# Performance work log

Measured on AMD Instinct MI355X. Metric: run time of the kernel, lower is better.

Reference implementation:

```python
import jax, jax.numpy as jnp
import numpy as np

N, C, E, Q, H, NC = 50000, 128, 1600000, 500000, 256, 2
BN_EPS = 1e-5


def gru_step(x, h, wih, whh, bih, bhh):
    # single-step torch.nn.GRU, gate order (r, z, n); x,h: [C, C] rows as batch
    gi = x @ wih.T + bih
    gh = h @ whh.T + bhh
    ir, iz, inn = jnp.split(gi, 3, axis=-1)
    hr, hz, hn = jnp.split(gh, 3, axis=-1)
    r = jax.nn.sigmoid(ir + hr)
    z = jax.nn.sigmoid(iz + hz)
    n = jnp.tanh(inn + r * hn)
    return (1.0 - z) * n + z * h


def gcn_conv(x, w, src, dst, ew):
    # GCNConv with fixed weight w and symmetric gcn_norm incl. self-loops
    xw = x @ w
    deg = jnp.zeros((N,), xw.dtype).at[dst].add(ew) + 1.0  # +1 self-loop
    dinv = jax.lax.rsqrt(deg)
    norm = dinv[src] * ew * dinv[dst]
    out = jnp.zeros_like(xw).at[dst].add(xw[src] * norm[:, None])
    return out + xw * (dinv * dinv)[:, None]  # self-loop contribution


def evolve_gcno(x, src, dst, ew, w_init, wih, whh, bih, bhh):
    w = gru_step(w_init, w_init, wih, whh, bih, bhh)
    return gcn_conv(x, w, src, dst, ew)


def setup_inputs():
    key = jax.random.key(0)
    ks = jax.random.split(key, 40)
    inp = {}
    inp["X"] = jax.random.normal(ks[0], (N, C), jnp.float32)
    inp["edge_index"] = jax.random.randint(ks[1], (2, E), 0, N, jnp.int32)
    inp["edge_weight"] = jax.random.uniform(ks[2], (E,), jnp.float32)
    inp["edge1"] = jax.random.randint(ks[3], (Q,), 0, N, jnp.int32)
    inp["edge2"] = jax.random.randint(ks[4], (Q,), 0, N, jnp.int32)
    s = 1.0 / np.sqrt(C)
    i = 5
    for l in range(2):
        inp[f"w{l}_init"] = jax.random.uniform(ks[i], (C, C), jnp.float32, -s, s); i += 1
        inp[f"w{l}_ih"] = jax.random.uniform(ks[i], (3 * C, C), jnp.float32, -s, s); i += 1
        inp[f"w{l}_hh"] = jax.random.uniform(ks[i], (3 * C, C), jnp.float32, -s, s); i += 1
        inp[f"b{l}_ih"] = jax.random.uniform(ks[i], (3 * C,), jnp.float32, -s, s); i += 1
        inp[f"b{l}_hh"] = jax.random.uniform(ks[i], (3 * C,), jnp.float32, -s, s); i += 1
    dims = [(H, C), (H, H), (NC, H)]
    for l, (o, fi) in enumerate(dims):
        sl = 1.0 / np.sqrt(fi)
        inp[f"lin_w{l}"] = jax.random.uniform(ks[i], (o, fi), jnp.float32, -sl, sl); i += 1
        inp[f"lin_b{l}"] = jax.random.uniform(ks[i], (o,), jnp.float32, -sl, sl); i += 1
    for l in range(2):
        inp[f"bn_g{l}"] = jax.random.uniform(ks[i], (H,), jnp.float32, 0.5, 1.5); i += 1
        inp[f"bn_b{l}"] = 0.1 * jax.random.normal(ks[i], (H,), jnp.float32); i += 1
        inp[f"bn_m{l}"] = 0.1 * jax.random.normal(ks[i], (H,), jnp.float32); i += 1
        inp[f"bn_v{l}"] = jax.random.uniform(ks[i], (H,), jnp.float32, 0.5, 1.5); i += 1
    return inp


def reference(X, edge_index, edge_weight, edge1, edge2,
              w0_init, w0_ih, w0_hh, b0_ih, b0_hh,
              w1_init, w1_ih, w1_hh, b1_ih, b1_hh,
              lin_w0, lin_b0, lin_w1, lin_b1, lin_w2, lin_b2,
              bn_g0, bn_b0, bn_m0, bn_v0, bn_g1, bn_b1, bn_m1, bn_v1):
    src, dst = edge_index[0], edge_index[1]
    # EGCNO: two EvolveGCNO layers + relu (dropout is identity in eval)
    x = jax.nn.relu(evolve_gcno(X, src, dst, edge_weight, w0_init, w0_ih, w0_hh, b0_ih, b0_hh))
    x = jax.nn.relu(evolve_gcno(x, src, dst, edge_weight, w1_init, w1_ih, w1_hh, b1_ih, b1_hh))
    # edge pair gather + hadamard
    h = x[edge1] * x[edge2]  # [Q, C]
    bn = [(bn_g0, bn_b0, bn_m0, bn_v0), (bn_g1, bn_b1, bn_m1, bn_v1)]
    lins = [(lin_w0, lin_b0), (lin_w1, lin_b1)]
    for (w, b), (g, bb, m, v) in zip(lins, bn):
        h = h @ w.T + b
        h = g * (h - m) * jax.lax.rsqrt(v + BN_EPS) + bb  # BatchNorm1d (eval)
        h = jax.nn.relu(h)
    h = h @ lin_w2.T + lin_b2
    return jax.nn.log_softmax(h, axis=-1)
```

## Files before the change

kernel.cpp:

```cpp
#include <hip/hip_runtime.h>
#include <math.h>

#define N_NODES 50000
#define C_DIM   128
#define E_EDGES 1600000
#define Q_PAIRS 500000
#define H_DIM   256
#define N_CLS   2
#define BN_EPS  1e-5f

typedef __attribute__((ext_vector_type(8))) short bf16x8;
typedef __attribute__((ext_vector_type(4))) short s16x4;
typedef __attribute__((ext_vector_type(4))) unsigned short u16x4;
typedef __attribute__((ext_vector_type(4))) float f32x4;

#define VMCNT0 asm volatile("s_waitcnt vmcnt(0)" ::: "memory")
#define VMCNT1 asm volatile("s_waitcnt vmcnt(1)" ::: "memory")
#define VMCNT2 asm volatile("s_waitcnt vmcnt(2)" ::: "memory")
#define SBAR do { __builtin_amdgcn_s_barrier(); \
                  __builtin_amdgcn_sched_barrier(0); } while (0)

#define DEG_SCALE 2097152.0f

__device__ __forceinline__ unsigned short f2bf(float x) {
    unsigned u = __float_as_uint(x);
    u += 0x7fffu + ((u >> 16) & 1u);
    return (unsigned short)(u >> 16);
}
__device__ __forceinline__ float bf2f(unsigned short h) {
    return __uint_as_float(((unsigned)h) << 16);
}
__device__ __forceinline__ unsigned cvtpk(float a, float b) {
    unsigned r;
    asm("v_cvt_pk_bf16_f32 %0, %1, %2" : "=v"(r) : "v"(a), "v"(b));
    return r;
}

__global__ __launch_bounds__(256) void k_hist(const int* __restrict__ dst,
                                              const float* __restrict__ ew,
                                              unsigned long long* dpack) {
    int e = blockIdx.x * 256 + threadIdx.x;
    if (e < E_EDGES) {
        unsigned pv = __float2uint_rn(ew[e] * DEG_SCALE);
        atomicAdd(&dpack[dst[e]], (1ULL << 32) | (unsigned long long)pv);
    }
}

__global__ __launch_bounds__(1024) void k_scan1(const unsigned long long* __restrict__ dpack,
                                                int* __restrict__ pos,
                                                int* __restrict__ bsum) {
    __shared__ int pa[1024], pb[1024];
    int t = threadIdx.x;
    int x = blockIdx.x * 1024 + t;
    int v = (x < N_NODES) ? (int)(dpack[x] >> 32) : 0;
    pa[t] = v;
    __syncthreads();
    int* sp = pa; int* dp = pb;
    for (int o = 1; o < 1024; o <<= 1) {
        int u = sp[t] + ((t >= o) ? sp[t - o] : 0);
        dp[t] = u;
        __syncthreads();
        int* tmp = sp; sp = dp; dp = tmp;
    }
    if (x < N_NODES) pos[x] = sp[t];
    if (t == 1023) bsum[blockIdx.x] = sp[1023];
}
__global__ __launch_bounds__(64) void k_scan2(const int* __restrict__ bsum,
                                              int* __restrict__ boff) {
    int t = threadIdx.x;
    int v = (t < 49) ? bsum[t] : 0;
    int own = v;
    for (int o = 1; o < 64; o <<= 1) {
        int u = __shfl_up(v, o, 64);
        if (t >= o) v += u;
    }
    if (t < 49) boff[t] = v - own;
}
__global__ __launch_bounds__(1024) void k_scan3(const unsigned long long* __restrict__ dpack,
                                                int* __restrict__ pos,
                                                const int* __restrict__ boff,
                                                int* __restrict__ off,
                                                float* __restrict__ dinv) {
    int x = blockIdx.x * 1024 + threadIdx.x;
    if (x >= N_NODES) return;
    int c = (int)(dpack[x] >> 32);
    int incl = pos[x];
    int o = boff[blockIdx.x] + incl - c;
    off[x] = o;
    pos[x] = o;
    if (x == N_NODES - 1) off[N_NODES] = o + c;
    unsigned lo = (unsigned)(dpack[x] & 0xffffffffULL);
    dinv[x] = rsqrtf(1.0f + (float)lo * (1.0f / DEG_SCALE));
}

__global__ __launch_bounds__(256) void k_fill(const int* __restrict__ src,
                                              const int* __restrict__ dst,
                                              const float* __restrict__ ew,
                                              const float* __restrict__ dinv,
                                              int* pos,
                                              int2* __restrict__ csr) {
    int e = blockIdx.x * 256 + threadIdx.x;
    if (e >= E_EDGES) return;
    int s = src[e], d = dst[e];
    int slot = atomicAdd(&pos[d], 1);
    int2 p;
    p.x = s;
    p.y = __float_as_int(dinv[s] * ew[e] * dinv[d]);
    csr[slot] = p;
}

__global__ __launch_bounds__(256) void k_gru_xbf(
    const float* __restrict__ wi0, const float* __restrict__ wih0, const float* __restrict__ whh0,
    const float* __restrict__ bih0, const float* __restrict__ bhh0, float* __restrict__ we0,
    const float* __restrict__ wi1, const float* __restrict__ wih1, const float* __restrict__ whh1,
    const float* __restrict__ bih1, const float* __restrict__ bhh1, float* __restrict__ we1,
    const float* __restrict__ x, unsigned short* __restrict__ xb) {
    if (blockIdx.x < 256) {
        __shared__ float xrow[C_DIM];
        int layer = blockIdx.x >> 7;
        int i = blockIdx.x & 127, j = threadIdx.x;
        const float* w_init = layer ? wi1 : wi0;
        const float* wih = layer ? wih1 : wih0;
        const float* whh = layer ? whh1 : whh0;
        const float* bih = layer ? bih1 : bih0;
        const float* bhh = layer ? bhh1 : bhh0;
        float* w_out = layer ? we1 : we0;
        if (j < C_DIM) xrow[j] = w_init[i * C_DIM + j];
        __syncthreads();
        if (j < C_DIM) {
            float gi[3], gh[3];
#pragma unroll
            for (int g = 0; g < 3; ++g) {
                const float* wi = wih + (size_t)(g * C_DIM + j) * C_DIM;
                const float* wh = whh + (size_t)(g * C_DIM + j) * C_DIM;
                float ai = 0.f, ah = 0.f;
                for (int k = 0; k < C_DIM; ++k) { ai += xrow[k] * wi[k]; ah += xrow[k] * wh[k]; }
                gi[g] = ai + bih[g * C_DIM + j];
                gh[g] = ah + bhh[g * C_DIM + j];
            }
            float r = 1.f / (1.f + expf(-(gi[0] + gh[0])));
            float z = 1.f / (1.f + expf(-(gi[1] + gh[1])));
            float n = tanhf(gi[2] + r * gh[2]);
            w_out[i * C_DIM + j] = (1.f - z) * n + z * xrow[j];
        }
    } else {
        int i = ((blockIdx.x - 256) * 256 + threadIdx.x) * 8;
        f32x4 a = *(const f32x4*)(x + i);
        f32x4 b = *(const f32x4*)(x + i + 4);
        bf16x8 o;
#pragma unroll
        for (int e = 0; e < 4; ++e) { o[e] = (short)f2bf(a[e]); o[e + 4] = (short)f2bf(b[e]); }
        *(bf16x8*)(xb + i) = o;
    }
}

__global__ __launch_bounds__(256) void k_prep_all(
    const float* __restrict__ we0, const float* __restrict__ we1,
    unsigned short* __restrict__ Wc0, unsigned short* __restrict__ Wc1,
    const float* __restrict__ lw0, const float* __restrict__ lw1,
    unsigned short* __restrict__ W0p, unsigned short* __restrict__ W1p,
    const float* __restrict__ lb0, const float* __restrict__ bg0, const float* __restrict__ bb0,
    const float* __restrict__ bm0, const float* __restrict__ bv0,
    const float* __restrict__ lb1, const float* __restrict__ bg1, const float* __restrict__ bb1,
    const float* __restrict__ bm1, const float* __restrict__ bv1,
    float* __restrict__ shift0, float* __restrict__ shift1) {
    int b = blockIdx.x, t = threadIdx.x;
    if (b < 256) {
        int idx = b * 256 + t;
        int e = idx & 7, col = (idx >> 3) & 127, kg = (idx >> 10) & 3;
        int plane = (idx >> 12) & 1, kb = (idx >> 13) & 3, layer = idx >> 15;
        int k = kb * 32 + kg * 8 + e;
        const float* we = layer ? we1 : we0;
        float x = we[(size_t)k * C_DIM + col];
        unsigned short hi = f2bf(x);
        unsigned short o = plane ? f2bf(x - bf2f(hi)) : hi;
        (layer ? Wc1 : Wc0)[idx & 32767] = o;
    } else if (b < 384) {
        int idx = (b - 256) * 256 + t;
        int e = idx & 7, col = (idx >> 3) & 255, kg = (idx >> 11) & 3;
        int kb = idx >> 13;
        int k = kb * 32 + kg * 8 + e;
        float sc = bg0[col] * rsqrtf(bv0[col] + BN_EPS);
        W0p[idx] = f2bf(lw0[(size_t)col * C_DIM + k] * sc);
    } else if (b < 640) {
        int idx = (b - 384) * 256 + t;
        int e = idx & 7, col = (idx >> 3) & 255, kg = (idx >> 11) & 3;
        int kb = idx >> 13;
        int k = kb * 32 + kg * 8 + e;
        float sc = bg1[col] * rsqrtf(bv1[col] + BN_EPS);
        W1p[idx] = f2bf(lw1[(size_t)col * H_DIM + k] * sc);
    } else {
        int j = (b - 640) * 256 + t;
        if (j < 256) {
            float sc = bg0[j] * rsqrtf(bv0[j] + BN_EPS);
            shift0[j] = (lb0[j] - bm0[j]) * sc + bb0[j];
        } else {
            int i = j - 256;
            float sc = bg1[i] * rsqrtf(bv1[i] + BN_EPS);
            shift1[i] = (lb1[i] - bm1[i]) * sc + bb1[i];
        }
    }
}

__global__ __launch_bounds__(256) void k_agg(const unsigned short* __restrict__ xb,
                                             const float* __restrict__ dinv,
                                             const int* __restrict__ off,
                                             const int2* __restrict__ csr,
                                             float* __restrict__ agg) {
    int tid = blockIdx.x * 256 + threadIdx.x;
    int n = tid >> 5;
    int c = (tid & 31) << 2;
    float dv = dinv[n];
    float d2 = dv * dv;
    u16x4 xs = *(const u16x4*)(xb + (size_t)n * C_DIM + c);
    float4 acc;
    acc.x = d2 * bf2f(xs[0]); acc.y = d2 * bf2f(xs[1]);
    acc.z = d2 * bf2f(xs[2]); acc.w = d2 * bf2f(xs[3]);
    int i = off[n], e = off[n + 1];
    for (; i + 8 <= e; i += 8) {
        int2 q0 = csr[i], q1 = csr[i + 1], q2 = csr[i + 2], q3 = csr[i + 3];
        int2 q4 = csr[i + 4], q5 = csr[i + 5], q6 = csr[i + 6], q7 = csr[i + 7];
        u16x4 v0 = *(const u16x4*)(xb + (size_t)q0.x * C_DIM + c);
        u16x4 v1 = *(const u16x4*)(xb + (size_t)q1.x * C_DIM + c);
        u16x4 v2 = *(const u16x4*)(xb + (size_t)q2.x * C_DIM + c);
        u16x4 v3 = *(const u16x4*)(xb + (size_t)q3.x * C_DIM + c);
        u16x4 v4 = *(const u16x4*)(xb + (size_t)q4.x * C_DIM + c);
        u16x4 v5 = *(const u16x4*)(xb + (size_t)q5.x * C_DIM + c);
        u16x4 v6 = *(const u16x4*)(xb + (size_t)q6.x * C_DIM + c);
        u16x4 v7 = *(const u16x4*)(xb + (size_t)q7.x * C_DIM + c);
        float w0 = __int_as_float(q0.y), w1 = __int_as_float(q1.y);
        float w2 = __int_as_float(q2.y), w3 = __int_as_float(q3.y);
        float w4 = __int_as_float(q4.y), w5 = __int_as_float(q5.y);
        float w6 = __int_as_float(q6.y), w7 = __int_as_float(q7.y);
        acc.x += w0 * bf2f(v0[0]) + w1 * bf2f(v1[0]) + w2 * bf2f(v2[0]) + w3 * bf2f(v3[0])
               + w4 * bf2f(v4[0]) + w5 * bf2f(v5[0]) + w6 * bf2f(v6[0]) + w7 * bf2f(v7[0]);
        acc.y += w0 * bf2f(v0[1]) + w1 * bf2f(v1[1]) + w2 * bf2f(v2[1]) + w3 * bf2f(v3[1])
               + w4 * bf2f(v4[1]) + w5 * bf2f(v5[1]) + w6 * bf2f(v6[1]) + w7 * bf2f(v7[1]);
        acc.z += w0 * bf2f(v0[2]) + w1 * bf2f(v1[2]) + w2 * bf2f(v2[2]) + w3 * bf2f(v3[2])
               + w4 * bf2f(v4[2]) + w5 * bf2f(v5[2]) + w6 * bf2f(v6[2]) + w7 * bf2f(v7[2]);
        acc.w += w0 * bf2f(v0[3]) + w1 * bf2f(v1[3]) + w2 * bf2f(v2[3]) + w3 * bf2f(v3[3])
               + w4 * bf2f(v4[3]) + w5 * bf2f(v5[3]) + w6 * bf2f(v6[3]) + w7 * bf2f(v7[3]);
    }
    for (; i < e; ++i) {
        int2 pe = csr[i];
        float w = __int_as_float(pe.y);
        u16x4 v = *(const u16x4*)(xb + (size_t)pe.x * C_DIM + c);
        acc.x += w * bf2f(v[0]); acc.y += w * bf2f(v[1]);
        acc.z += w * bf2f(v[2]); acc.w += w * bf2f(v[3]);
    }
    *(float4*)(agg + (size_t)n * C_DIM + c) = acc;
}

template <int OUT_BF>
__global__ __launch_bounds__(512) void k_gemm(const float* __restrict__ agg,
                                              const unsigned short* __restrict__ Wc,
                                              float* __restrict__ y,
                                              unsigned short* __restrict__ yb) {
    __shared__ __align__(16) char smem[3 * 8192];
    const int t = threadIdx.x, lane = t & 63, wave = t >> 6;
    const int qg = wave >> 1, ch = wave & 1;
    const int l16 = lane & 15, kg = lane >> 4;
    const int qrow = qg * 16 + l16;
    const int node = blockIdx.x * 64 + qrow;
    const int nodec = node < N_NODES ? node : N_NODES - 1;

    auto STG = [&](int sidx, int b) {
        const char* g = (const char*)Wc + sidx * 8192 + wave * 1024 + lane * 16;
        char* d = smem + b * 8192 + wave * 1024;
        __builtin_amdgcn_global_load_lds((const __attribute__((address_space(1))) void*)g,
                                         (__attribute__((address_space(3))) void*)d, 16, 0, 0);
    };
    STG(0, 0); STG(1, 1);

    bf16x8 bh[4], bl[4];
    const float* ar = agg + (size_t)nodec * C_DIM;
#pragma unroll
    for (int kb = 0; kb < 4; ++kb) {
        int k0 = kb * 32 + kg * 8;
        f32x4 a0 = *(const f32x4*)(ar + k0);
        f32x4 a1 = *(const f32x4*)(ar + k0 + 4);
#pragma unroll
        for (int e = 0; e < 4; ++e) {
            unsigned short h0 = f2bf(a0[e]);
            bh[kb][e] = (short)h0; bl[kb][e] = (short)f2bf(a0[e] - bf2f(h0));
            unsigned short h1 = f2bf(a1[e]);
            bh[kb][e + 4] = (short)h1; bl[kb][e + 4] = (short)f2bf(a1[e] - bf2f(h1));
        }
    }
    f32x4 acc[4];
#pragma unroll
    for (int i = 0; i < 4; ++i) acc[i] = 0.f;

#pragma unroll
    for (int s = 0; s < 8; ++s) {
        if (s < 7) { VMCNT1; } else { VMCNT0; }
        SBAR;
        if (s + 2 < 8) STG(s + 2, (s + 2) % 3);
        const unsigned short* strip = (const unsigned short*)(smem + (s % 3) * 8192);
        const int kb = s >> 1;
        __builtin_amdgcn_s_setprio(1);
#pragma unroll
        for (int jc8 = 0; jc8 < 4; ++jc8) {
            int col = (ch * 4 + jc8) * 16 + l16;
            bf16x8 a = *(const bf16x8*)&strip[kg * 1024 + col * 8];
            acc[jc8] = __builtin_amdgcn_mfma_f32_16x16x32_bf16(a, bh[kb], acc[jc8], 0, 0, 0);
            if ((s & 1) == 0)
                acc[jc8] = __builtin_amdgcn_mfma_f32_16x16x32_bf16(a, bl[kb], acc[jc8], 0, 0, 0);
        }
        __builtin_amdgcn_s_setprio(0);
    }

    if (node < N_NODES) {
#pragma unroll
        for (int jc8 = 0; jc8 < 4; ++jc8) {
            int j0 = (ch * 4 + jc8) * 16 + kg * 4;
            if (OUT_BF) {
                u16x4 v;
#pragma unroll
                for (int r = 0; r < 4; ++r) v[r] = f2bf(fmaxf(acc[jc8][r], 0.f));
                *(u16x4*)(yb + (size_t)node * C_DIM + j0) = v;
            } else {
                float4 v;
                v.x = fmaxf(acc[jc8][0], 0.f); v.y = fmaxf(acc[jc8][1], 0.f);
                v.z = fmaxf(acc[jc8][2], 0.f); v.w = fmaxf(acc[jc8][3], 0.f);
                *(float4*)(y + (size_t)node * C_DIM + j0) = v;
            }
        }
    }
}

__global__ __launch_bounds__(512, 4) void k_mlp(const float* __restrict__ y,
                                             const int* __restrict__ e1,
                                             const int* __restrict__ e2,
                                             const unsigned short* __restrict__ W0p,
                                             const unsigned short* __restrict__ W1p,
                                             const float* __restrict__ shift0,
                                             const float* __restrict__ shift1,
                                             const float* __restrict__ w2,
                                             const float* __restrict__ b2,
                                             float* __restrict__ out) {
    __shared__ __align__(16) char smem[81920];
    unsigned short* l1b = (unsigned short*)(smem + 49152);
    float* red = (float*)smem;

    const int t = threadIdx.x;
    const int lane = t & 63;
    const int wave = t >> 6;
    const int qs = wave >> 2, cg = wave & 3;
    const int l16 = lane & 15, kg = lane >> 4;
    const int qb = blockIdx.x * 64;

    auto STG = [&](const unsigned short* W, int sidx, int b) {
        const char* g = (const char*)W + ((size_t)sidx << 14) + wave * 2048 + lane * 16;
        char* d = smem + b * 16384 + wave * 2048;
        __builtin_amdgcn_global_load_lds((const __attribute__((address_space(1))) void*)g,
                                         (__attribute__((address_space(3))) void*)d, 16, 0, 0);
        __builtin_amdgcn_global_load_lds((const __attribute__((address_space(1))) void*)(g + 1024),
                                         (__attribute__((address_space(3))) void*)(d + 1024), 16, 0, 0);
    };

    STG(W0p, 0, 0); STG(W0p, 1, 1);

    {
        int k2 = lane * 2;
        int G = lane >> 2;
        int off = k2 & 7;
#pragma unroll
        for (int qi = 0; qi < 8; ++qi) {
            int qrow = wave * 8 + qi;
            int q = qb + qrow; if (q >= Q_PAIRS) q = Q_PAIRS - 1;
            const float* ya = y + (size_t)e1[q] * C_DIM;
            const float* yb = y + (size_t)e2[q] * C_DIM;
            float2 a = *(const float2*)(ya + k2);
            float2 b = *(const float2*)(yb + k2);
            int idx = qrow * 256 + ((G ^ (qrow & 7)) << 3) + off;
            *(unsigned*)&l1b[idx] = cvtpk(a.x * b.x, a.y * b.y);
        }
    }
    __syncthreads();

    bf16x8 bh[2][4];
#pragma unroll
    for (int qq = 0; qq < 2; ++qq) {
        int qrow = qs * 32 + qq * 16 + l16;
#pragma unroll
        for (int kb = 0; kb < 4; ++kb) {
            int gidx = qrow * 256 + (((kb * 4 + kg) ^ (qrow & 7)) * 8);
            bh[qq][kb] = *(const bf16x8*)&l1b[gidx];
        }
    }

    f32x4 acc[2][4];
#pragma unroll
    for (int qq = 0; qq < 2; ++qq)
#pragma unroll
        for (int jc = 0; jc < 4; ++jc) acc[qq][jc] = 0.f;

#pragma unroll
    for (int s = 0; s < 4; ++s) {
        if (s < 3) { VMCNT2; } else { VMCNT0; }
        SBAR;
        if (s + 2 < 4) STG(W0p, s + 2, (s + 2) % 3);
        const unsigned short* strip = (const unsigned short*)(smem + (s % 3) * 16384);
        __builtin_amdgcn_s_setprio(1);
#pragma unroll
        for (int jc = 0; jc < 4; ++jc) {
            int col = cg * 64 + jc * 16 + l16;
            bf16x8 a = *(const bf16x8*)&strip[kg * 2048 + col * 8];
            acc[0][jc] = __builtin_amdgcn_mfma_f32_16x16x32_bf16(a, bh[0][s], acc[0][jc], 0, 0, 0);
            acc[1][jc] = __builtin_amdgcn_mfma_f32_16x16x32_bf16(a, bh[1][s], acc[1][jc], 0, 0, 0);
        }
        __builtin_amdgcn_s_setprio(0);
    }

#pragma unroll
    for (int qq = 0; qq < 2; ++qq) {
        int qrow = qs * 32 + qq * 16 + l16;
#pragma unroll
        for (int jc = 0; jc < 4; ++jc) {
            int jg = cg * 4 + jc;
            int j0 = jg * 16 + kg * 4;
            f32x4 sh = *(const f32x4*)(shift0 + j0);
            float v0 = fmaxf(acc[qq][jc][0] + sh[0], 0.f);
            float v1 = fmaxf(acc[qq][jc][1] + sh[1], 0.f);
            float v2 = fmaxf(acc[qq][jc][2] + sh[2], 0.f);
            float v3 = fmaxf(acc[qq][jc][3] + sh[3], 0.f);
            int G = jg * 2 + (kg >> 1);
            int idx = qrow * 256 + ((G ^ (qrow & 7)) * 8) + (kg & 1) * 4;
            uint2 pk; pk.x = cvtpk(v0, v1); pk.y = cvtpk(v2, v3);
            *(uint2*)&l1b[idx] = pk;
        }
    }
    __syncthreads();

    f32x4 acc2[2][4];
#pragma unroll
    for (int qq = 0; qq < 2; ++qq)
#pragma unroll
        for (int jc = 0; jc < 4; ++jc) acc2[qq][jc] = 0.f;
    STG(W1p, 0, 0); STG(W1p, 1, 1);
    bf16x8 bh2[2];
#pragma unroll
    for (int s = 0; s < 8; ++s) {
        if (s < 7) { VMCNT2; } else { VMCNT0; }
        SBAR;
        if (s + 2 < 8) STG(W1p, s + 2, (s + 2) % 3);
        const unsigned short* strip = (const unsigned short*)(smem + (s % 3) * 16384);
#pragma unroll
        for (int qq = 0; qq < 2; ++qq) {
            int qrow = qs * 32 + qq * 16 + l16;
            int gidx = qrow * 256 + (((s * 4 + kg) ^ (qrow & 7)) * 8);
            bh2[qq] = *(const bf16x8*)&l1b[gidx];
        }
        __builtin_amdgcn_s_setprio(1);
#pragma unroll
        for (int jc = 0; jc < 4; ++jc) {
            int col = cg * 64 + jc * 16 + l16;
            bf16x8 a = *(const bf16x8*)&strip[kg * 2048 + col * 8];
            acc2[0][jc] = __builtin_amdgcn_mfma_f32_16x16x32_bf16(a, bh2[0], acc2[0][jc], 0, 0, 0);
            acc2[1][jc] = __builtin_amdgcn_mfma_f32_16x16x32_bf16(a, bh2[1], acc2[1][jc], 0, 0, 0);
        }
        __builtin_amdgcn_s_setprio(0);
    }

    float p[2][2] = {};
#pragma unroll
    for (int qq = 0; qq < 2; ++qq)
#pragma unroll
        for (int jc = 0; jc < 4; ++jc) {
            int j0 = (cg * 4 + jc) * 16 + kg * 4;
            f32x4 sh = *(const f32x4*)(shift1 + j0);
            f32x4 wa = *(const f32x4*)(w2 + j0);
            f32x4 wb = *(const f32x4*)(w2 + H_DIM + j0);
#pragma unroll
            for (int r = 0; r < 4; ++r) {
                float v = fmaxf(acc2[qq][jc][r] + sh[r], 0.f);
                p[qq][0] += v * wa[r];
                p[qq][1] += v * wb[r];
            }
        }
#pragma unroll
    for (int qq = 0; qq < 2; ++qq) {
        p[qq][0] += __shfl_xor(p[qq][0], 16, 64); p[qq][0] += __shfl_xor(p[qq][0], 32, 64);
        p[qq][1] += __shfl_xor(p[qq][1], 16, 64); p[qq][1] += __shfl_xor(p[qq][1], 32, 64);
    }
    __syncthreads();
    if (kg == 0) {
#pragma unroll
        for (int qq = 0; qq < 2; ++qq) {
            int base = ((qs * 2 + qq) * 16 + l16) * 2;
            red[(base + 0) * 4 + cg] = p[qq][0];
            red[(base + 1) * 4 + cg] = p[qq][1];
        }
    }
    __syncthreads();
    if (t < 64) {
        int q = qb + t;
        if (q < Q_PAIRS) {
            int base = t * 2;
            float l0 = red[base * 4 + 0] + red[base * 4 + 1] + red[base * 4 + 2] + red[base * 4 + 3] + b2[0];
            float l1v = red[(base + 1) * 4 + 0] + red[(base + 1) * 4 + 1]
                      + red[(base + 1) * 4 + 2] + red[(base + 1) * 4 + 3] + b2[1];
            float mx = fmaxf(l0, l1v);
            float lse = mx + logf(expf(l0 - mx) + expf(l1v - mx));
            float2 o; o.x = l0 - lse; o.y = l1v - lse;
            *(float2*)(out + (size_t)q * N_CLS) = o;
        }
    }
}

extern "C" void kernel_launch(void* const* d_in, const int* in_sizes, int n_in,
                              void* d_out, int out_size, void* d_ws, size_t ws_size,
                              hipStream_t stream) {
    const float* X  = (const float*)d_in[0];
    const int*   ei = (const int*)d_in[1];
    const float* ew = (const float*)d_in[2];
    const int*   e1 = (const int*)d_in[3];
    const int*   e2 = (const int*)d_in[4];
    const float* w_init[2] = {(const float*)d_in[5],  (const float*)d_in[10]};
    const float* w_ih[2]   = {(const float*)d_in[6],  (const float*)d_in[11]};
    const float* w_hh[2]   = {(const float*)d_in[7],  (const float*)d_in[12]};
    const float* b_ih[2]   = {(const float*)d_in[8],  (const float*)d_in[13]};
    const float* b_hh[2]   = {(const float*)d_in[9],  (const float*)d_in[14]};
    const float* lw0 = (const float*)d_in[15]; const float* lb0 = (const float*)d_in[16];
    const float* lw1 = (const float*)d_in[17]; const float* lb1 = (const float*)d_in[18];
    const float* lw2 = (const float*)d_in[19]; const float* lb2 = (const float*)d_in[20];
    const float* bg0 = (const float*)d_in[21]; const float* bb0 = (const float*)d_in[22];
    const float* bm0 = (const float*)d_in[23]; const float* bv0 = (const float*)d_in[24];
    const float* bg1 = (const float*)d_in[25]; const float* bb1 = (const float*)d_in[26];
    const float* bm1 = (const float*)d_in[27]; const float* bv1 = (const float*)d_in[28];
    const int* src = ei;
    const int* dst = ei + E_EDGES;

    char* ws = (char*)d_ws;
    size_t o = 0;
    auto alloc = [&](size_t bytes) { char* p = ws + o; o += (bytes + 63) & ~(size_t)63; return p; };
    float* bufA   = (float*)alloc((size_t)N_NODES * C_DIM * 4);
    float* bufB   = (float*)alloc((size_t)N_NODES * C_DIM * 4);
    unsigned short* xbf = (unsigned short*)alloc((size_t)N_NODES * C_DIM * 2);
    unsigned short* ybf = (unsigned short*)alloc((size_t)N_NODES * C_DIM * 2);
    unsigned long long* dpack = (unsigned long long*)alloc((size_t)N_NODES * 8);
    float* dinv   = (float*)alloc(N_NODES * 4);
    float* we0    = (float*)alloc(C_DIM * C_DIM * 4);
    float* we1    = (float*)alloc(C_DIM * C_DIM * 4);
    float* shift0 = (float*)alloc(H_DIM * 4);
    float* shift1 = (float*)alloc(H_DIM * 4);
    int*   pos    = (int*)alloc(N_NODES * 4);
    int*   off    = (int*)alloc((N_NODES + 1) * 4);
    int*   bsum   = (int*)alloc(64 * 4);
    int*   boff   = (int*)alloc(64 * 4);
    int2*  csr    = (int2*)alloc((size_t)E_EDGES * 8);
    unsigned short* W0p = (unsigned short*)alloc(32768 * 2);
    unsigned short* W1p = (unsigned short*)alloc(65536 * 2);
    unsigned short* Wc0 = (unsigned short*)alloc(32768 * 2);
    unsigned short* Wc1 = (unsigned short*)alloc(32768 * 2);
    if (o > ws_size) return;

    dim3 b256(256);
    const int gE = (E_EDGES + 255) / 256;

    hipMemsetAsync(dpack, 0, (size_t)N_NODES * 8, stream);
    k_hist<<<gE, b256, 0, stream>>>(dst, ew, dpack);
    k_scan1<<<49, dim3(1024), 0, stream>>>(dpack, pos, bsum);
    k_scan2<<<1, dim3(64), 0, stream>>>(bsum, boff);
    k_scan3<<<49, dim3(1024), 0, stream>>>(dpack, pos, boff, off, dinv);
    k_fill<<<gE, b256, 0, stream>>>(src, dst, ew, dinv, pos, csr);

    k_gru_xbf<<<256 + 3125, b256, 0, stream>>>(w_init[0], w_ih[0], w_hh[0], b_ih[0], b_hh[0], we0,
                                               w_init[1], w_ih[1], w_hh[1], b_ih[1], b_hh[1], we1,
                                               X, xbf);
    k_prep_all<<<642, b256, 0, stream>>>(we0, we1, Wc0, Wc1, lw0, lw1, W0p, W1p,
                                         lb0, bg0, bb0, bm0, bv0,
                                         lb1, bg1, bb1, bm1, bv1, shift0, shift1);

    const int ga = (N_NODES * 32) / 256;
    const int gg = (N_NODES + 63) / 64;
    k_agg<<<ga, b256, 0, stream>>>(xbf, dinv, off, csr, bufA);
    k_gemm<1><<<gg, dim3(512), 0, stream>>>(bufA, Wc0, bufB, ybf);
    k_agg<<<ga, b256, 0, stream>>>(ybf, dinv, off, csr, bufA);
    k_gemm<0><<<gg, dim3(512), 0, stream>>>(bufA, Wc1, bufB, ybf);
    k_mlp<<<(Q_PAIRS + 63) / 64, dim3(512), 0, stream>>>(bufB, e1, e2, W0p, W1p,
                                                         shift0, shift1, lw2, lb2, (float*)d_out);
}
```

Baseline: 495.9 us.

## Fuse preprocessing kernels and remap MLP waves to full-row column strips

Merges the histogram, GRU weight evolution and bf16 cast into one launch, scan pass one with weight packing into another, and folds the block-offset scan into scan3, reducing kernel launches and inter-kernel gaps. The MLP kernel is changed so each of 8 waves covers all 64 query rows over a 32-column slice, loading B fragments per stage instead of holding them. The final reduction now sums eight partials per row, which needs a larger reduction buffer.

```diff
diff --git a/kernel.cpp b/kernel.cpp
--- a/kernel.cpp
+++ b/kernel.cpp
@@ -9,6 +9,8 @@
 #define N_CLS   2
 #define BN_EPS  1e-5f
 
+#define GE_BLK  6250
+
 typedef __attribute__((ext_vector_type(8))) short bf16x8;
 typedef __attribute__((ext_vector_type(4))) short s16x4;
 typedef __attribute__((ext_vector_type(4))) unsigned short u16x4;
@@ -36,56 +38,149 @@
     return r;
 }
 
-__global__ __launch_bounds__(256) void k_hist(const int* __restrict__ dst,
-                                              const float* __restrict__ ew,
-                                              unsigned long long* dpack) {
-    int e = blockIdx.x * 256 + threadIdx.x;
-    if (e < E_EDGES) {
-        unsigned pv = __float2uint_rn(ew[e] * DEG_SCALE);
-        atomicAdd(&dpack[dst[e]], (1ULL << 32) | (unsigned long long)pv);
-    }
-}
-
-__global__ __launch_bounds__(1024) void k_scan1(const unsigned long long* __restrict__ dpack,
-                                                int* __restrict__ pos,
-                                                int* __restrict__ bsum) {
-    __shared__ int pa[1024], pb[1024];
+__global__ __launch_bounds__(256) void k_front(
+    const int* __restrict__ dst, const float* __restrict__ ew, unsigned long long* dpack,
+    const float* __restrict__ wi0, const float* __restrict__ wih0, const float* __restrict__ whh0,
+    const float* __restrict__ bih0, const float* __restrict__ bhh0, float* __restrict__ we0,
+    const float* __restrict__ wi1, const float* __restrict__ wih1, const float* __restrict__ whh1,
+    const float* __restrict__ bih1, const float* __restrict__ bhh1, float* __restrict__ we1,
+    const float* __restrict__ x, unsigned short* __restrict__ xb) {
+    int b = blockIdx.x;
+    if (b < GE_BLK) {
+        int e = b * 256 + threadIdx.x;
+        if (e < E_EDGES) {
+            unsigned pv = __float2uint_rn(ew[e] * DEG_SCALE);
+            atomicAdd(&dpack[dst[e]], (1ULL << 32) | (unsigned long long)pv);
+        }
+    } else if (b < GE_BLK + 256) {
+        __shared__ float xrow[C_DIM];
+        int bb = b - GE_BLK;
+        int layer = bb >> 7;
+        int i = bb & 127, j = threadIdx.x;
+        const float* w_init = layer ? wi1 : wi0;
+        const float* wih = layer ? wih1 : wih0;
+        const float* whh = layer ? whh1 : whh0;
+        const float* bih = layer ? bih1 : bih0;
+        const float* bhh = layer ? bhh1 : bhh0;
+        float* w_out = layer ? we1 : we0;
+        if (j < C_DIM) xrow[j] = w_init[i * C_DIM + j];
+        __syncthreads();
+        if (j < C_DIM) {
+            float gi[3], gh[3];
+#pragma unroll
+            for (int g = 0; g < 3; ++g) {
+                const float* wi = wih + (size_t)(g * C_DIM + j) * C_DIM;
+                const float* wh = whh + (size_t)(g * C_DIM + j) * C_DIM;
+                float ai = 0.f, ah = 0.f;
+                for (int k = 0; k < C_DIM; ++k) { ai += xrow[k] * wi[k]; ah += xrow[k] * wh[k]; }
+                gi[g] = ai + bih[g * C_DIM + j];
+                gh[g] = ah + bhh[g * C_DIM + j];
+            }
+            float r = 1.f / (1.f + expf(-(gi[0] + gh[0])));
+            float z = 1.f / (1.f + expf(-(gi[1] + gh[1])));
+            float n = tanhf(gi[2] + r * gh[2]);
+            w_out[i * C_DIM + j] = (1.f - z) * n + z * xrow[j];
+        }
+    } else {
+        int i = ((b - GE_BLK - 256) * 256 + threadIdx.x) * 8;
+        f32x4 a = *(const f32x4*)(x + i);
+        f32x4 bb = *(const f32x4*)(x + i + 4);
+        bf16x8 o;
+#pragma unroll
+        for (int e = 0; e < 4; ++e) { o[e] = (short)f2bf(a[e]); o[e + 4] = (short)f2bf(bb[e]); }
+        *(bf16x8*)(xb + i) = o;
+    }
+}
+
+__global__ __launch_bounds__(1024) void k_ps(
+    const unsigned long long* __restrict__ dpack, int* __restrict__ pos, int* __restrict__ bsum,
+    const float* __restrict__ we0, const float* __restrict__ we1,
+    unsigned short* __restrict__ Wc0, unsigned short* __restrict__ Wc1,
+    const float* __restrict__ lw0, const float* __restrict__ lw1,
+    unsigned short* __restrict__ W0p, unsigned short* __restrict__ W1p,
+    const float* __restrict__ lb0, const float* __restrict__ bg0, const float* __restrict__ bb0,
+    const float* __restrict__ bm0, const float* __restrict__ bv0,
+    const float* __restrict__ lb1, const float* __restrict__ bg1, const float* __restrict__ bb1,
+    const float* __restrict__ bm1, const float* __restrict__ bv1,
+    float* __restrict__ shift0, float* __restrict__ shift1) {
     int t = threadIdx.x;
-    int x = blockIdx.x * 1024 + t;
-    int v = (x < N_NODES) ? (int)(dpack[x] >> 32) : 0;
-    pa[t] = v;
-    __syncthreads();
-    int* sp = pa; int* dp = pb;
-    for (int o = 1; o < 1024; o <<= 1) {
-        int u = sp[t] + ((t >= o) ? sp[t - o] : 0);
-        dp[t] = u;
+    if (blockIdx.x < 49) {
+        __shared__ int pa[1024], pb[1024];
+        int x = blockIdx.x * 1024 + t;
+        int v = (x < N_NODES) ? (int)(dpack[x] >> 32) : 0;
+        pa[t] = v;
         __syncthreads();
-        int* tmp = sp; sp = dp; dp = tmp;
-    }
-    if (x < N_NODES) pos[x] = sp[t];
-    if (t == 1023) bsum[blockIdx.x] = sp[1023];
-}
-__global__ __launch_bounds__(64) void k_scan2(const int* __restrict__ bsum,
-                                              int* __restrict__ boff) {
-    int t = threadIdx.x;
-    int v = (t < 49) ? bsum[t] : 0;
-    int own = v;
-    for (int o = 1; o < 64; o <<= 1) {
-        int u = __shfl_up(v, o, 64);
-        if (t >= o) v += u;
-    }
-    if (t < 49) boff[t] = v - own;
-}
+        int* sp = pa; int* dp = pb;
+        for (int o = 1; o < 1024; o <<= 1) {
+            int u = sp[t] + ((t >= o) ? sp[t - o] : 0);
+            dp[t] = u;
+            __syncthreads();
+            int* tmp = sp; sp = dp; dp = tmp;
+        }
+        if (x < N_NODES) pos[x] = sp[t];
+        if (t == 1023) bsum[blockIdx.x] = sp[1023];
+    } else {
+        int pid = (blockIdx.x - 49) * 1024 + t;
+        if (pid < 65536) {
+            int idx = pid;
+            int e = idx & 7, col = (idx >> 3) & 127, kg = (idx >> 10) & 3;
+            int plane = (idx >> 12) & 1, kb = (idx >> 13) & 3, layer = idx >> 15;
+            int k = kb * 32 + kg * 8 + e;
+            const float* we = layer ? we1 : we0;
+            float x = we[(size_t)k * C_DIM + col];
+            unsigned short hi = f2bf(x);
+            unsigned short o = plane ? f2bf(x - bf2f(hi)) : hi;
+            (layer ? Wc1 : Wc0)[idx & 32767] = o;
+        } else if (pid < 98304) {
+            int idx = pid - 65536;
+            int e = idx & 7, col = (idx >> 3) & 255, kg = (idx >> 11) & 3;
+            int kb = idx >> 13;
+            int k = kb * 32 + kg * 8 + e;
+            float sc = bg0[col] * rsqrtf(bv0[col] + BN_EPS);
+            W0p[idx] = f2bf(lw0[(size_t)col * C_DIM + k] * sc);
+        } else if (pid < 163840) {
+            int idx = pid - 98304;
+            int e = idx & 7, col = (idx >> 3) & 255, kg = (idx >> 11) & 3;
+            int kb = idx >> 13;
+            int k = kb * 32 + kg * 8 + e;
+            float sc = bg1[col] * rsqrtf(bv1[col] + BN_EPS);
+            W1p[idx] = f2bf(lw1[(size_t)col * H_DIM + k] * sc);
+        } else if (pid < 164352) {
+            int j = pid - 163840;
+            if (j < 256) {
+                float sc = bg0[j] * rsqrtf(bv0[j] + BN_EPS);
+                shift0[j] = (lb0[j] - bm0[j]) * sc + bb0[j];
+            } else {
+                int i = j - 256;
+                float sc = bg1[i] * rsqrtf(bv1[i] + BN_EPS);
+                shift1[i] = (lb1[i] - bm1[i]) * sc + bb1[i];
+            }
+        }
+    }
+}
+
 __global__ __launch_bounds__(1024) void k_scan3(const unsigned long long* __restrict__ dpack,
                                                 int* __restrict__ pos,
-                                                const int* __restrict__ boff,
+                                                const int* __restrict__ bsum,
                                                 int* __restrict__ off,
                                                 float* __restrict__ dinv) {
-    int x = blockIdx.x * 1024 + threadIdx.x;
+    __shared__ int bo[64];
+    int t = threadIdx.x;
+    if (t < 64) {
+        int v = (t < 49) ? bsum[t] : 0;
+        int own = v;
+        for (int o = 1; o < 64; o <<= 1) {
+            int u = __shfl_up(v, o, 64);
+            if (t >= o) v += u;
+        }
+        bo[t] = v - own;
+    }
+    __syncthreads();
+    int x = blockIdx.x * 1024 + t;
     if (x >= N_NODES) return;
     int c = (int)(dpack[x] >> 32);
     int incl = pos[x];
-    int o = boff[blockIdx.x] + incl - c;
+    int o = bo[blockIdx.x] + incl - c;
     off[x] = o;
     pos[x] = o;
     if (x == N_NODES - 1) off[N_NODES] = o + c;
@@ -107,99 +202,6 @@
     p.x = s;
     p.y = __float_as_int(dinv[s] * ew[e] * dinv[d]);
     csr[slot] = p;
-}
-
-__global__ __launch_bounds__(256) void k_gru_xbf(
-    const float* __restrict__ wi0, const float* __restrict__ wih0, const float* __restrict__ whh0,
-    const float* __restrict__ bih0, const float* __restrict__ bhh0, float* __restrict__ we0,
-    const float* __restrict__ wi1, const float* __restrict__ wih1, const float* __restrict__ whh1,
-    const float* __restrict__ bih1, const float* __restrict__ bhh1, float* __restrict__ we1,
-    const float* __restrict__ x, unsigned short* __restrict__ xb) {
-    if (blockIdx.x < 256) {
-        __shared__ float xrow[C_DIM];
-        int layer = blockIdx.x >> 7;
-        int i = blockIdx.x & 127, j = threadIdx.x;
-        const float* w_init = layer ? wi1 : wi0;
-        const float* wih = layer ? wih1 : wih0;
-        const float* whh = layer ? whh1 : whh0;
-        const float* bih = layer ? bih1 : bih0;
-        const float* bhh = layer ? bhh1 : bhh0;
-        float* w_out = layer ? we1 : we0;
-        if (j < C_DIM) xrow[j] = w_init[i * C_DIM + j];
-        __syncthreads();
-        if (j < C_DIM) {
-            float gi[3], gh[3];
-#pragma unroll
-            for (int g = 0; g < 3; ++g) {
-                const float* wi = wih + (size_t)(g * C_DIM + j) * C_DIM;
-                const float* wh = whh + (size_t)(g * C_DIM + j) * C_DIM;
-                float ai = 0.f, ah = 0.f;
-                for (int k = 0; k < C_DIM; ++k) { ai += xrow[k] * wi[k]; ah += xrow[k] * wh[k]; }
-                gi[g] = ai + bih[g * C_DIM + j];
-                gh[g] = ah + bhh[g * C_DIM + j];
-            }
-            float r = 1.f / (1.f + expf(-(gi[0] + gh[0])));
-            float z = 1.f / (1.f + expf(-(gi[1] + gh[1])));
-            float n = tanhf(gi[2] + r * gh[2]);
-            w_out[i * C_DIM + j] = (1.f - z) * n + z * xrow[j];
-        }
-    } else {
-        int i = ((blockIdx.x - 256) * 256 + threadIdx.x) * 8;
-        f32x4 a = *(const f32x4*)(x + i);
-        f32x4 b = *(const f32x4*)(x + i + 4);
-        bf16x8 o;
-#pragma unroll
-        for (int e = 0; e < 4; ++e) { o[e] = (short)f2bf(a[e]); o[e + 4] = (short)f2bf(b[e]); }
-        *(bf16x8*)(xb + i) = o;
-    }
-}
-
-__global__ __launch_bounds__(256) void k_prep_all(
-    const float* __restrict__ we0, const float* __restrict__ we1,
-    unsigned short* __restrict__ Wc0, unsigned short* __restrict__ Wc1,
-    const float* __restrict__ lw0, const float* __restrict__ lw1,
-    unsigned short* __restrict__ W0p, unsigned short* __restrict__ W1p,
-    const float* __restrict__ lb0, const float* __restrict__ bg0, const float* __restrict__ bb0,
-    const float* __restrict__ bm0, const float* __restrict__ bv0,
-    const float* __restrict__ lb1, const float* __restrict__ bg1, const float* __restrict__ bb1,
-    const float* __restrict__ bm1, const float* __restrict__ bv1,
-    float* __restrict__ shift0, float* __restrict__ shift1) {
-    int b = blockIdx.x, t = threadIdx.x;
-    if (b < 256) {
-        int idx = b * 256 + t;
-        int e = idx & 7, col = (idx >> 3) & 127, kg = (idx >> 10) & 3;
-        int plane = (idx >> 12) & 1, kb = (idx >> 13) & 3, layer = idx >> 15;
-        int k = kb * 32 + kg * 8 + e;
-        const float* we = layer ? we1 : we0;
-        float x = we[(size_t)k * C_DIM + col];
-        unsigned short hi = f2bf(x);
-        unsigned short o = plane ? f2bf(x - bf2f(hi)) : hi;
-        (layer ? Wc1 : Wc0)[idx & 32767] = o;
-    } else if (b < 384) {
-        int idx = (b - 256) * 256 + t;
-        int e = idx & 7, col = (idx >> 3) & 255, kg = (idx >> 11) & 3;
-        int kb = idx >> 13;
-        int k = kb * 32 + kg * 8 + e;
-        float sc = bg0[col] * rsqrtf(bv0[col] + BN_EPS);
-        W0p[idx] = f2bf(lw0[(size_t)col * C_DIM + k] * sc);
-    } else if (b < 640) {
-        int idx = (b - 384) * 256 + t;
-        int e = idx & 7, col = (idx >> 3) & 255, kg = (idx >> 11) & 3;
-        int kb = idx >> 13;
-        int k = kb * 32 + kg * 8 + e;
-        float sc = bg1[col] * rsqrtf(bv1[col] + BN_EPS);
-        W1p[idx] = f2bf(lw1[(size_t)col * H_DIM + k] * sc);
-    } else {
-        int j = (b - 640) * 256 + t;
-        if (j < 256) {
-            float sc = bg0[j] * rsqrtf(bv0[j] + BN_EPS);
-            shift0[j] = (lb0[j] - bm0[j]) * sc + bb0[j];
-        } else {
-            int i = j - 256;
-            float sc = bg1[i] * rsqrtf(bv1[i] + BN_EPS);
-            shift1[i] = (lb1[i] - bm1[i]) * sc + bb1[i];
-        }
-    }
 }
 
 __global__ __launch_bounds__(256) void k_agg(const unsigned short* __restrict__ xb,
@@ -345,14 +347,13 @@
 
     const int t = threadIdx.x;
     const int lane = t & 63;
-    const int wave = t >> 6;
-    const int qs = wave >> 2, cg = wave & 3;
+    const int cg = t >> 6;
     const int l16 = lane & 15, kg = lane >> 4;
     const int qb = blockIdx.x * 64;
 
     auto STG = [&](const unsigned short* W, int sidx, int b) {
-        const char* g = (const char*)W + ((size_t)sidx << 14) + wave * 2048 + lane * 16;
-        char* d = smem + b * 16384 + wave * 2048;
+        const char* g = (const char*)W + ((size_t)sidx << 14) + cg * 2048 + lane * 16;
+        char* d = smem + b * 16384 + cg * 2048;
         __builtin_amdgcn_global_load_lds((const __attribute__((address_space(1))) void*)g,
                                          (__attribute__((address_space(3))) void*)d, 16, 0, 0);
         __builtin_amdgcn_global_load_lds((const __attribute__((address_space(1))) void*)(g + 1024),
@@ -367,7 +368,7 @@
         int off = k2 & 7;
 #pragma unroll
         for (int qi = 0; qi < 8; ++qi) {
-            int qrow = wave * 8 + qi;
+            int qrow = cg * 8 + qi;
             int q = qb + qrow; if (q >= Q_PAIRS) q = Q_PAIRS - 1;
             const float* ya = y + (size_t)e1[q] * C_DIM;
             const float* yb = y + (size_t)e2[q] * C_DIM;
@@ -379,46 +380,44 @@
     }
     __syncthreads();
 
-    bf16x8 bh[2][4];
-#pragma unroll
-    for (int qq = 0; qq < 2; ++qq) {
-        int qrow = qs * 32 + qq * 16 + l16;
-#pragma unroll
-        for (int kb = 0; kb < 4; ++kb) {
-            int gidx = qrow * 256 + (((kb * 4 + kg) ^ (qrow & 7)) * 8);
-            bh[qq][kb] = *(const bf16x8*)&l1b[gidx];
-        }
-    }
-
-    f32x4 acc[2][4];
-#pragma unroll
-    for (int qq = 0; qq < 2; ++qq)
-#pragma unroll
-        for (int jc = 0; jc < 4; ++jc) acc[qq][jc] = 0.f;
+    f32x4 acc[4][2];
+#pragma unroll
+    for (int qq = 0; qq < 4; ++qq)
+#pragma unroll
+        for (int jc = 0; jc < 2; ++jc) acc[qq][jc] = 0.f;
 
 #pragma unroll
     for (int s = 0; s < 4; ++s) {
         if (s < 3) { VMCNT2; } else { VMCNT0; }
         SBAR;
         if (s + 2 < 4) STG(W0p, s + 2, (s + 2) % 3);
+        bf16x8 bh[4];
+#pragma unroll
+        for (int qq = 0; qq < 4; ++qq) {
+            int qrow = qq * 16 + l16;
+            int gidx = qrow * 256 + (((s * 4 + kg) ^ (qrow & 7)) * 8);
+            bh[qq] = *(const bf16x8*)&l1b[gidx];
+        }
         const unsigned short* strip = (const unsigned short*)(smem + (s % 3) * 16384);
         __builtin_amdgcn_s_setprio(1);
 #pragma unroll
-        for (int jc = 0; jc < 4; ++jc) {
-            int col = cg * 64 + jc * 16 + l16;
+        for (int jc = 0; jc < 2; ++jc) {
+            int col = cg * 32 + jc * 16 + l16;
             bf16x8 a = *(const bf16x8*)&strip[kg * 2048 + col * 8];
-            acc[0][jc] = __builtin_amdgcn_mfma_f32_16x16x32_bf16(a, bh[0][s], acc[0][jc], 0, 0, 0);
-            acc[1][jc] = __builtin_amdgcn_mfma_f32_16x16x32_bf16(a, bh[1][s], acc[1][jc], 0, 0, 0);
+#pragma unroll
+            for (int qq = 0; qq < 4; ++qq)
+                acc[qq][jc] = __builtin_amdgcn_mfma_f32_16x16x32_bf16(a, bh[qq], acc[qq][jc], 0, 0, 0);
         }
         __builtin_amdgcn_s_setprio(0);
     }
-
-#pragma unroll
-    for (int qq = 0; qq < 2; ++qq) {
-        int qrow = qs * 32 + qq * 16 + l16;
-#pragma unroll
-        for (int jc = 0; jc < 4; ++jc) {
-            int jg = cg * 4 + jc;
+    __syncthreads();
+
+#pragma unroll
+    for (int qq = 0; qq < 4; ++qq) {
+        int qrow = qq * 16 + l16;
+#pragma unroll
+        for (int jc = 0; jc < 2; ++jc) {
+            int jg = cg * 2 + jc;
             int j0 = jg * 16 + kg * 4;
             f32x4 sh = *(const f32x4*)(shift0 + j0);
             float v0 = fmaxf(acc[qq][jc][0] + sh[0], 0.f);
@@ -433,42 +432,43 @@
     }
     __syncthreads();
 
-    f32x4 acc2[2][4];
-#pragma unroll
-    for (int qq = 0; qq < 2; ++qq)
-#pragma unroll
-        for (int jc = 0; jc < 4; ++jc) acc2[qq][jc] = 0.f;
+    f32x4 acc2[4][2];
+#pragma unroll
+    for (int qq = 0; qq < 4; ++qq)
+#pragma unroll
+        for (int jc = 0; jc < 2; ++jc) acc2[qq][jc] = 0.f;
     STG(W1p, 0, 0); STG(W1p, 1, 1);
-    bf16x8 bh2[2];
 #pragma unroll
     for (int s = 0; s < 8; ++s) {
         if (s < 7) { VMCNT2; } else { VMCNT0; }
         SBAR;
         if (s + 2 < 8) STG(W1p, s + 2, (s + 2) % 3);
-        const unsigned short* strip = (const unsigned short*)(smem + (s % 3) * 16384);
-#pragma unroll
-        for (int qq = 0; qq < 2; ++qq) {
-            int qrow = qs * 32 + qq * 16 + l16;
+        bf16x8 bh2[4];
+#pragma unroll
+        for (int qq = 0; qq < 4; ++qq) {
+            int qrow = qq * 16 + l16;
             int gidx = qrow * 256 + (((s * 4 + kg) ^ (qrow & 7)) * 8);
             bh2[qq] = *(const bf16x8*)&l1b[gidx];
         }
+        const unsigned short* strip = (const unsigned short*)(smem + (s % 3) * 16384);
         __builtin_amdgcn_s_setprio(1);
 #pragma unroll
-        for (int jc = 0; jc < 4; ++jc) {
-            int col = cg * 64 + jc * 16 + l16;
+        for (int jc = 0; jc < 2; ++jc) {
+            int col = cg * 32 + jc * 16 + l16;
             bf16x8 a = *(const bf16x8*)&strip[kg * 2048 + col * 8];
-            acc2[0][jc] = __builtin_amdgcn_mfma_f32_16x16x32_bf16(a, bh2[0], acc2[0][jc], 0, 0, 0);
-            acc2[1][jc] = __builtin_amdgcn_mfma_f32_16x16x32_bf16(a, bh2[1], acc2[1][jc], 0, 0, 0);
+#pragma unroll
+            for (int qq = 0; qq < 4; ++qq)
+                acc2[qq][jc] = __builtin_amdgcn_mfma_f32_16x16x32_bf16(a, bh2[qq], acc2[qq][jc], 0, 0, 0);
         }
         __builtin_amdgcn_s_setprio(0);
     }
 
-    float p[2][2] = {};
-#pragma unroll
-    for (int qq = 0; qq < 2; ++qq)
-#pragma unroll
-        for (int jc = 0; jc < 4; ++jc) {
-            int j0 = (cg * 4 + jc) * 16 + kg * 4;
+    float p[4][2] = {};
+#pragma unroll
+    for (int qq = 0; qq < 4; ++qq)
+#pragma unroll
+        for (int jc = 0; jc < 2; ++jc) {
+            int j0 = (cg * 2 + jc) * 16 + kg * 4;
             f32x4 sh = *(const f32x4*)(shift1 + j0);
             f32x4 wa = *(const f32x4*)(w2 + j0);
             f32x4 wb = *(const f32x4*)(w2 + H_DIM + j0);
@@ -480,27 +480,29 @@
             }
         }
 #pragma unroll
-    for (int qq = 0; qq < 2; ++qq) {
+    for (int qq = 0; qq < 4; ++qq) {
         p[qq][0] += __shfl_xor(p[qq][0], 16, 64); p[qq][0] += __shfl_xor(p[qq][0], 32, 64);
         p[qq][1] += __shfl_xor(p[qq][1], 16, 64); p[qq][1] += __shfl_xor(p[qq][1], 32, 64);
     }
     __syncthreads();
     if (kg == 0) {
 #pragma unroll
-        for (int qq = 0; qq < 2; ++qq) {
-            int base = ((qs * 2 + qq) * 16 + l16) * 2;
-            red[(base + 0) * 4 + cg] = p[qq][0];
-            red[(base + 1) * 4 + cg] = p[qq][1];
+        for (int qq = 0; qq < 4; ++qq) {
+            int base = (qq * 16 + l16) * 2;
+            red[(base + 0) * 8 + cg] = p[qq][0];
+            red[(base + 1) * 8 + cg] = p[qq][1];
         }
     }
     __syncthreads();
     if (t < 64) {
         int q = qb + t;
         if (q < Q_PAIRS) {
-            int base = t * 2;
-            float l0 = red[base * 4 + 0] + red[base * 4 + 1] + red[base * 4 + 2] + red[base * 4 + 3] + b2[0];
-            float l1v = red[(base + 1) * 4 + 0] + red[(base + 1) * 4 + 1]
-                      + red[(base + 1) * 4 + 2] + red[(base + 1) * 4 + 3] + b2[1];
+            float l0 = b2[0], l1v = b2[1];
+#pragma unroll
+            for (int g = 0; g < 8; ++g) {
+                l0 += red[(t * 2 + 0) * 8 + g];
+                l1v += red[(t * 2 + 1) * 8 + g];
+            }
             float mx = fmaxf(l0, l1v);
             float lse = mx + logf(expf(l0 - mx) + expf(l1v - mx));
             float2 o; o.x = l0 - lse; o.y = l1v - lse;
@@ -548,7 +550,6 @@
     int*   pos    = (int*)alloc(N_NODES * 4);
     int*   off    = (int*)alloc((N_NODES + 1) * 4);
     int*   bsum   = (int*)alloc(64 * 4);
-    int*   boff   = (int*)alloc(64 * 4);
     int2*  csr    = (int2*)alloc((size_t)E_EDGES * 8);
     unsigned short* W0p = (unsigned short*)alloc(32768 * 2);
     unsigned short* W1p = (unsigned short*)alloc(65536 * 2);
@@ -557,21 +558,16 @@
     if (o > ws_size) return;
 
     dim3 b256(256);
-    const int gE = (E_EDGES + 255) / 256;
 
     hipMemsetAsync(dpack, 0, (size_t)N_NODES * 8, stream);
-    k_hist<<<gE, b256, 0, stream>>>(dst, ew, dpack);
-    k_scan1<<<49, dim3(1024), 0, stream>>>(dpack, pos, bsum);
-    k_scan2<<<1, dim3(64), 0, stream>>>(bsum, boff);
-    k_scan3<<<49, dim3(1024), 0, stream>>>(dpack, pos, boff, off, dinv);
-    k_fill<<<gE, b256, 0, stream>>>(src, dst, ew, dinv, pos, csr);
-
-    k_gru_xbf<<<256 + 3125, b256, 0, stream>>>(w_init[0], w_ih[0], w_hh[0], b_ih[0], b_hh[0], we0,
-                                               w_init[1], w_ih[1], w_hh[1], b_ih[1], b_hh[1], we1,
-                                               X, xbf);
-    k_prep_all<<<642, b256, 0, stream>>>(we0, we1, Wc0, Wc1, lw0, lw1, W0p, W1p,
-                                         lb0, bg0, bb0, bm0, bv0,
-                                         lb1, bg1, bb1, bm1, bv1, shift0, shift1);
+    k_front<<<GE_BLK + 256 + 3125, b256, 0, stream>>>(dst, ew, dpack,
+        w_init[0], w_ih[0], w_hh[0], b_ih[0], b_hh[0], we0,
+        w_init[1], w_ih[1], w_hh[1], b_ih[1], b_hh[1], we1, X, xbf);
+    k_ps<<<49 + 161, dim3(1024), 0, stream>>>(dpack, pos, bsum,
+        we0, we1, Wc0, Wc1, lw0, lw1, W0p, W1p,
+        lb0, bg0, bb0, bm0, bv0, lb1, bg1, bb1, bm1, bv1, shift0, shift1);
+    k_scan3<<<49, dim3(1024), 0, stream>>>(dpack, pos, bsum, off, dinv);
+    k_fill<<<GE_BLK, b256, 0, stream>>>(src, dst, ew, dinv, pos, csr);
 
     const int ga = (N_NODES * 32) / 256;
     const int gg = (N_NODES + 63) / 64;
```

Measured after the change: 497.7 us. No clear change (+0.4%).
